# Performance work log

Hardware: AMD Instinct MI355X
Metric: run time of the kernel (lower is better)

The kernel has to match this reference:

```python
import jax, jax.numpy as jnp
import numpy as np

B, S, E, H = 4, 1024, 1024, 16
D = E // H  # head_dim = 64
SCALE = float(np.sqrt(D))


def setup_inputs() -> dict:
    key = jax.random.key(0)
    ks = jax.random.split(key, 12)
    lim = 1.0 / np.sqrt(E)  # torch nn.Linear default init range

    def lin(kw, kb):
        W = jax.random.uniform(kw, (E, E), jnp.float32, -lim, lim)
        b = jax.random.uniform(kb, (E,), jnp.float32, -lim, lim)
        return W, b

    W0, b0 = lin(ks[0], ks[1])
    W1, b1 = lin(ks[2], ks[3])
    W2, b2 = lin(ks[4], ks[5])
    Wv, bv = lin(ks[6], ks[7])
    Wo, bo = lin(ks[8], ks[9])
    A = jax.random.normal(ks[10], (D, D, D), jnp.float32)  # torch.randn core tensor
    x = jax.random.normal(ks[11], (B, S, E), jnp.float32)
    return {"x": x, "W0": W0, "b0": b0, "W1": W1, "b1": b1, "W2": W2, "b2": b2,
            "Wv": Wv, "bv": bv, "Wo": Wo, "bo": bo, "A": A}


def _heads(h):
    # (B,S,E) -> (B,H,S,D)
    return h.reshape(B, S, H, D).transpose(0, 2, 1, 3)


def reference(x, W0, b0, W1, b1, W2, b2, Wv, bv, Wo, bo, A):
    p0 = _heads(x @ W0.T + b0)
    p1 = _heads(x @ W1.T + b1)
    p2 = _heads(x @ W2.T + b2)
    # N=3 multilinear attention score: third projection is contracted over its
    # own sequence index k (faithful to the original einsum construction).
    logits = jnp.einsum('acd,bhia,bhjc,bhkd->bhij', A, p0, p1, p2,
                        optimize=True) / SCALE  # (B,H,S,S)
    attn = jax.nn.softmax(logits, axis=-1)  # dropout inactive (eval / p=0)
    v = _heads(x @ Wv.T + bv)
    values = jnp.einsum('bhij,bhjd->bhid', attn, v)  # (B,H,S,D)
    values = values.transpose(0, 2, 1, 3).reshape(B, S, E)
    out = values @ Wo.T + bo
    return out, attn
```

## Files before the change

kernel.cpp:

```cpp
#include <hip/hip_runtime.h>
#include <hip/hip_bf16.h>
#include <cstddef>

#define B_ 4
#define S_ 1024
#define E_ 1024
#define H_ 16
#define D_ 64
#define BH_ (B_*H_)

typedef __attribute__((ext_vector_type(8))) short short8;
typedef __attribute__((ext_vector_type(4))) float f32x4;
typedef __attribute__((ext_vector_type(4))) unsigned short us4;
typedef unsigned short u16;

__device__ inline u16 f2b(float x) {
    return __builtin_bit_cast(u16, __float2bfloat16(x));
}
__device__ inline float b2f(u16 u) {
    return __bfloat162float(__builtin_bit_cast(__hip_bfloat16, u));
}
__device__ inline void splitf(float x, u16& h, u16& l) {
    h = f2b(x); l = f2b(x - b2f(h));
}

__device__ inline void split_one(const float* __restrict__ in,
                                 u16* __restrict__ oh, u16* __restrict__ ol, int i)
{
    float4 v = ((const float4*)in)[i];
    us4 h, l;
    splitf(v.x, ((u16*)&h)[0], ((u16*)&l)[0]);
    splitf(v.y, ((u16*)&h)[1], ((u16*)&l)[1]);
    splitf(v.z, ((u16*)&h)[2], ((u16*)&l)[2]);
    splitf(v.w, ((u16*)&h)[3], ((u16*)&l)[3]);
    ((us4*)oh)[i] = h;
    ((us4*)ol)[i] = l;
}

__global__ __launch_bounds__(256) void prep(
    const float* __restrict__ x, const float* __restrict__ W0,
    const float* __restrict__ W1, float* __restrict__ xsum_p,
    u16* __restrict__ xh, u16* __restrict__ xl,
    u16* __restrict__ w0h, u16* __restrict__ w0l,
    u16* __restrict__ w1h, u16* __restrict__ w1l)
{
    int bid = blockIdx.x, tid = threadIdx.x;
    if (bid < 4096) {
        split_one(x, xh, xl, bid * 256 + tid);
    } else if (bid < 5120) {
        split_one(W0, w0h, w0l, (bid - 4096) * 256 + tid);
    } else if (bid < 6144) {
        split_one(W1, w1h, w1l, (bid - 5120) * 256 + tid);
    } else {
        int p = bid - 6144;
        int kb = p & 3, b = (p >> 2) & 3, ch = p >> 4;
        int k = kb * 256 + tid;
        const float* base = x + ((size_t)(b * S_ + ch * 64)) * E_ + k;
        float s = 0.f;
#pragma unroll 8
        for (int j = 0; j < 64; ++j) s += base[(size_t)j * E_];
        xsum_p[(ch * 4 + b) * E_ + k] = s;
    }
}

__global__ __launch_bounds__(256) void t2k_M(
    const float* __restrict__ W2, const float* __restrict__ b2v,
    const float* __restrict__ xsum_p, const float* __restrict__ A,
    u16* __restrict__ MTh, u16* __restrict__ MTl)
{
    int h = blockIdx.x, b = blockIdx.y, tid = threadIdx.x;
    __shared__ float xs[1024];
    __shared__ float t2s[64];

#pragma unroll
    for (int j = 0; j < 4; ++j) {
        int k = j * 256 + tid;
        float s = 0.f;
#pragma unroll
        for (int c = 0; c < 16; ++c) s += xsum_p[(c * 4 + b) * E_ + k];
        xs[k] = s;
    }
    __syncthreads();

    int w = tid >> 6, lane = tid & 63;
    for (int nn = w; nn < 64; nn += 4) {
        int n = h * 64 + nn;
        const float* wr = W2 + (size_t)n * E_;
        float s = 0.f;
#pragma unroll
        for (int t = 0; t < 16; ++t) s = fmaf(wr[t * 64 + lane], xs[t * 64 + lane], s);
#pragma unroll
        for (int off = 1; off < 64; off <<= 1) s += __shfl_xor(s, off, 64);
        if (lane == 0) t2s[nn] = s + 1024.0f * b2v[n];
    }
    __syncthreads();

    int bh = b * H_ + h;
    int c = tid & 63;
    int a0 = (tid >> 6) * 16;
    for (int a = a0; a < a0 + 16; ++a) {
        float s = 0.f;
        const float* Ap = A + ((size_t)a * 64 + c) * 64;
#pragma unroll 8
        for (int d = 0; d < 64; ++d) s = fmaf(Ap[d], t2s[d], s);
        u16 hh, ll; splitf(s * 0.125f, hh, ll);
        MTh[(size_t)bh * 4096 + c * 64 + a] = hh;
        MTl[(size_t)bh * 4096 + c * 64 + a] = ll;
    }
}

__global__ __launch_bounds__(256) void gemm_qp1(
    const u16* __restrict__ Xh, const u16* __restrict__ Xl,
    const u16* __restrict__ W0h_, const u16* __restrict__ W0l_,
    const u16* __restrict__ W1h_, const u16* __restrict__ W1l_,
    const float* __restrict__ bias0, const float* __restrict__ bias1,
    const u16* __restrict__ MTh, const u16* __restrict__ MTl,
    u16* __restrict__ qh, u16* __restrict__ ql,
    u16* __restrict__ p1h, u16* __restrict__ p1l)
{
    const int K = 1024;
    __shared__ __align__(16) char smem[40960];
    u16* Xs_h  = (u16*)smem;
    u16* Xs_l  = Xs_h + 128 * 40;
    u16* W0s_h = Xs_l + 128 * 40;
    u16* W0s_l = W0s_h + 64 * 40;
    u16* W1s_h = W0s_l + 64 * 40;
    u16* W1s_l = W1s_h + 64 * 40;
    u16* Cs_h  = (u16*)smem;
    u16* Cs_l  = Cs_h + 128 * 72;

    const int tid = threadIdx.x;
    const int w = tid >> 6, lane = tid & 63;
    const int waveM = w & 1, waveN = w >> 1;
    const int quad = lane >> 4, l16 = lane & 15;
    const int bm = blockIdx.x, bn = blockIdx.y;

    const int xrow = tid >> 1, xko = (tid & 1) * 16;
    const int wrow = tid >> 2, wko = (tid & 3) * 8;

    const u16* xh_g  = Xh  + (size_t)(bm * 128 + xrow) * K + xko;
    const u16* xl_g  = Xl  + (size_t)(bm * 128 + xrow) * K + xko;
    const u16* w0h_g = W0h_ + (size_t)(bn * 64 + wrow) * K + wko;
    const u16* w0l_g = W0l_ + (size_t)(bn * 64 + wrow) * K + wko;
    const u16* w1h_g = W1h_ + (size_t)(bn * 64 + wrow) * K + wko;
    const u16* w1l_g = W1l_ + (size_t)(bn * 64 + wrow) * K + wko;

    f32x4 acc0[4][2] = {};
    f32x4 acc1[4][2] = {};

    for (int k0 = 0; k0 < K; k0 += 32) {
        uint4 xa = *(const uint4*)(xh_g + k0);
        uint4 xb = *(const uint4*)(xh_g + k0 + 8);
        uint4 xc = *(const uint4*)(xl_g + k0);
        uint4 xd = *(const uint4*)(xl_g + k0 + 8);
        uint4 w0a = *(const uint4*)(w0h_g + k0);
        uint4 w0c = *(const uint4*)(w0l_g + k0);
        uint4 w1a = *(const uint4*)(w1h_g + k0);
        uint4 w1c = *(const uint4*)(w1l_g + k0);
        __syncthreads();
        *(uint4*)&Xs_h[xrow * 40 + xko]     = xa;
        *(uint4*)&Xs_h[xrow * 40 + xko + 8] = xb;
        *(uint4*)&Xs_l[xrow * 40 + xko]     = xc;
        *(uint4*)&Xs_l[xrow * 40 + xko + 8] = xd;
        *(uint4*)&W0s_h[wrow * 40 + wko] = w0a;
        *(uint4*)&W0s_l[wrow * 40 + wko] = w0c;
        *(uint4*)&W1s_h[wrow * 40 + wko] = w1a;
        *(uint4*)&W1s_l[wrow * 40 + wko] = w1c;
        __syncthreads();

        short8 ah[4], al[4], b0h[2], b0l[2], b1h[2], b1l[2];
#pragma unroll
        for (int mt = 0; mt < 4; ++mt) {
            int r = (waveM * 64 + mt * 16 + l16) * 40 + quad * 8;
            ah[mt] = *(short8*)&Xs_h[r];
            al[mt] = *(short8*)&Xs_l[r];
        }
#pragma unroll
        for (int nt = 0; nt < 2; ++nt) {
            int r = (waveN * 32 + nt * 16 + l16) * 40 + quad * 8;
            b0h[nt] = *(short8*)&W0s_h[r];
            b0l[nt] = *(short8*)&W0s_l[r];
            b1h[nt] = *(short8*)&W1s_h[r];
            b1l[nt] = *(short8*)&W1s_l[r];
        }
#pragma unroll
        for (int mt = 0; mt < 4; ++mt)
#pragma unroll
            for (int nt = 0; nt < 2; ++nt) {
                acc0[mt][nt] = __builtin_amdgcn_mfma_f32_16x16x32_bf16(ah[mt], b0h[nt], acc0[mt][nt], 0, 0, 0);
                acc1[mt][nt] = __builtin_amdgcn_mfma_f32_16x16x32_bf16(ah[mt], b1h[nt], acc1[mt][nt], 0, 0, 0);
                acc0[mt][nt] = __builtin_amdgcn_mfma_f32_16x16x32_bf16(ah[mt], b0l[nt], acc0[mt][nt], 0, 0, 0);
                acc1[mt][nt] = __builtin_amdgcn_mfma_f32_16x16x32_bf16(ah[mt], b1l[nt], acc1[mt][nt], 0, 0, 0);
                acc0[mt][nt] = __builtin_amdgcn_mfma_f32_16x16x32_bf16(al[mt], b0h[nt], acc0[mt][nt], 0, 0, 0);
                acc1[mt][nt] = __builtin_amdgcn_mfma_f32_16x16x32_bf16(al[mt], b1h[nt], acc1[mt][nt], 0, 0, 0);
            }
    }

    const int bh = (bm >> 3) * H_ + bn;

#pragma unroll
    for (int mt = 0; mt < 4; ++mt)
#pragma unroll
        for (int nt = 0; nt < 2; ++nt)
#pragma unroll
            for (int r = 0; r < 4; ++r) {
                int m = bm * 128 + waveM * 64 + mt * 16 + quad * 4 + r;
                int n = bn * 64 + waveN * 32 + nt * 16 + l16;
                float val = acc1[mt][nt][r] + bias1[n];
                int s = m & 1023, c = n & 63;
                size_t addr = ((size_t)bh * S_ + s) * 64 + c;
                u16 hh, ll; splitf(val, hh, ll);
                p1h[addr] = hh; p1l[addr] = ll;
            }

    __syncthreads();
#pragma unroll
    for (int mt = 0; mt < 4; ++mt)
#pragma unroll
        for (int nt = 0; nt < 2; ++nt)
#pragma unroll
            for (int r = 0; r < 4; ++r) {
                int i = waveM * 64 + mt * 16 + quad * 4 + r;
                int a = waveN * 32 + nt * 16 + l16;
                float val = acc0[mt][nt][r] + bias0[bn * 64 + a];
                u16 hh, ll; splitf(val, hh, ll);
                Cs_h[i * 72 + a] = hh;
                Cs_l[i * 72 + a] = ll;
            }
    __syncthreads();

    const u16* MTh_b = MTh + (size_t)bh * 4096;
    const u16* MTl_b = MTl + (size_t)bh * 4096;
    f32x4 qacc[4][2] = {};
#pragma unroll
    for (int ch = 0; ch < 2; ++ch) {
        short8 mh[2], ml[2];
#pragma unroll
        for (int nt = 0; nt < 2; ++nt) {
            int c = waveN * 32 + nt * 16 + l16;
            mh[nt] = *(const short8*)&MTh_b[c * 64 + ch * 32 + quad * 8];
            ml[nt] = *(const short8*)&MTl_b[c * 64 + ch * 32 + quad * 8];
        }
#pragma unroll
        for (int mt = 0; mt < 4; ++mt) {
            int rr = (waveM * 64 + mt * 16 + l16) * 72 + ch * 32 + quad * 8;
            short8 ca = *(short8*)&Cs_h[rr];
            short8 cl = *(short8*)&Cs_l[rr];
#pragma unroll
            for (int nt = 0; nt < 2; ++nt) {
                qacc[mt][nt] = __builtin_amdgcn_mfma_f32_16x16x32_bf16(ca, mh[nt], qacc[mt][nt], 0, 0, 0);
                qacc[mt][nt] = __builtin_amdgcn_mfma_f32_16x16x32_bf16(ca, ml[nt], qacc[mt][nt], 0, 0, 0);
                qacc[mt][nt] = __builtin_amdgcn_mfma_f32_16x16x32_bf16(cl, mh[nt], qacc[mt][nt], 0, 0, 0);
            }
        }
    }
#pragma unroll
    for (int mt = 0; mt < 4; ++mt)
#pragma unroll
        for (int nt = 0; nt < 2; ++nt)
#pragma unroll
            for (int r = 0; r < 4; ++r) {
                int s = (bm & 7) * 128 + waveM * 64 + mt * 16 + quad * 4 + r;
                int c = waveN * 32 + nt * 16 + l16;
                size_t addr = ((size_t)bh * S_ + s) * 64 + c;
                u16 hh, ll; splitf(qacc[mt][nt][r], hh, ll);
                qh[addr] = hh; ql[addr] = ll;
            }
}

__global__ __launch_bounds__(256) void gemm_plain(
    const u16* __restrict__ Xb, const float* __restrict__ Wf,
    const float* __restrict__ bias, u16* __restrict__ outB,
    float* __restrict__ outF, int mode)
{
    const int K = 1024;
    __shared__ __align__(16) u16 Xs[64 * 40];
    __shared__ __align__(16) u16 Ws[64 * 40];

    const int tid = threadIdx.x;
    const int w = tid >> 6, lane = tid & 63;
    const int waveM = w & 1, waveN = w >> 1;
    const int quad = lane >> 4, l16 = lane & 15;
    const int bm = blockIdx.x, bn = blockIdx.y;
    const int lrow = tid >> 2, lkoff = (tid & 3) * 8;

    const u16* xg = Xb + (size_t)(bm * 64 + lrow) * K + lkoff;
    const float* wg = Wf + (size_t)(bn * 64 + lrow) * K + lkoff;

    f32x4 acc[2][2] = {};

    for (int k0 = 0; k0 < K; k0 += 32) {
        uint4 xv = *(const uint4*)(xg + k0);
        float4 w0 = *(const float4*)(wg + k0);
        float4 w1 = *(const float4*)(wg + k0 + 4);
        short8 wp;
        ((u16*)&wp)[0] = f2b(w0.x); ((u16*)&wp)[1] = f2b(w0.y);
        ((u16*)&wp)[2] = f2b(w0.z); ((u16*)&wp)[3] = f2b(w0.w);
        ((u16*)&wp)[4] = f2b(w1.x); ((u16*)&wp)[5] = f2b(w1.y);
        ((u16*)&wp)[6] = f2b(w1.z); ((u16*)&wp)[7] = f2b(w1.w);
        __syncthreads();
        *(uint4*)&Xs[lrow * 40 + lkoff] = xv;
        *(short8*)&Ws[lrow * 40 + lkoff] = wp;
        __syncthreads();

        short8 af[2], bf_[2];
#pragma unroll
        for (int mt = 0; mt < 2; ++mt)
            af[mt] = *(short8*)&Xs[(waveM * 32 + mt * 16 + l16) * 40 + quad * 8];
#pragma unroll
        for (int nt = 0; nt < 2; ++nt)
            bf_[nt] = *(short8*)&Ws[(waveN * 32 + nt * 16 + l16) * 40 + quad * 8];
#pragma unroll
        for (int mt = 0; mt < 2; ++mt)
#pragma unroll
            for (int nt = 0; nt < 2; ++nt)
                acc[mt][nt] = __builtin_amdgcn_mfma_f32_16x16x32_bf16(af[mt], bf_[nt], acc[mt][nt], 0, 0, 0);
    }

#pragma unroll
    for (int mt = 0; mt < 2; ++mt)
#pragma unroll
        for (int nt = 0; nt < 2; ++nt)
#pragma unroll
            for (int r = 0; r < 4; ++r) {
                int m = bm * 64 + waveM * 32 + mt * 16 + quad * 4 + r;
                int n = bn * 64 + waveN * 32 + nt * 16 + l16;
                float val = acc[mt][nt][r] + bias[n];
                if (mode == 0) {
                    int b = m >> 10, s = m & 1023, h = n >> 6, c = n & 63;
                    outB[((size_t)((b * H_ + h) * 64 + c)) * S_ + s] = f2b(val);
                } else {
                    outF[(size_t)m * 1024 + n] = val;
                }
            }
}

__global__ __launch_bounds__(512) void logits_softmax_pv(
    const u16* __restrict__ qh, const u16* __restrict__ ql,
    const u16* __restrict__ p1h, const u16* __restrict__ p1l,
    const u16* __restrict__ vT, float* __restrict__ attn,
    u16* __restrict__ values)
{
    int bh = blockIdx.x, i0 = blockIdx.y * 32;
    int b = bh >> 4, h = bh & 15;
    int tid = threadIdx.x, w = tid >> 6, lane = tid & 63;
    int quad = lane >> 4, l16 = lane & 15;
    int wg = w >> 2, wj = w & 3;

    __shared__ __align__(16) char sm[60928];
    u16* qhs  = (u16*)sm;
    u16* qls  = (u16*)(sm + 4608);
    u16* p1hs = (u16*)(sm + 9216);
    u16* p1ls = (u16*)(sm + 27648);
    float* redm = (float*)(sm + 46080);
    float* reds = (float*)(sm + 46592);
    u16* Ps  = (u16*)(sm + 9216);
    u16* vs_ = (u16*)(sm + 18432);

    {
        int row = tid >> 4, c0 = (tid & 15) * 4;
        size_t g = ((size_t)bh * S_ + i0 + row) * 64 + c0;
        *(us4*)&qhs[row * 72 + c0] = *(const us4*)&qh[g];
        *(us4*)&qls[row * 72 + c0] = *(const us4*)&ql[g];
    }

    const int jl = tid >> 3, c0s = (tid & 7) * 8;
    const size_t gp = ((size_t)bh * S_ + jl) * 64 + c0s;

    uint4 rha = *(const uint4*)&p1h[gp];
    uint4 rla = *(const uint4*)&p1l[gp];
    *(uint4*)&p1hs[jl * 72 + c0s] = rha;
    *(uint4*)&p1ls[jl * 72 + c0s] = rla;
    uint4 rh1 = *(const uint4*)&p1h[gp + 4096];
    uint4 rl1 = *(const uint4*)&p1l[gp + 4096];
    __syncthreads();

    short8 ah[2], al[2];
#pragma unroll
    for (int ch = 0; ch < 2; ++ch) {
        ah[ch] = *(short8*)&qhs[(wg * 16 + l16) * 72 + ch * 32 + quad * 8];
        al[ch] = *(short8*)&qls[(wg * 16 + l16) * 72 + ch * 32 + quad * 8];
    }

    f32x4 L[16];
    for (int t = 0; t < 16; ++t) {
        int cur = t & 1;
        uint4 rh2, rl2;
        if (t < 14) {
            size_t gn = gp + (size_t)(t + 2) * 4096;
            rh2 = *(const uint4*)&p1h[gn];
            rl2 = *(const uint4*)&p1l[gn];
        }
        int jr = wj * 16 + l16;
        const u16* Hb = &p1hs[cur * 4608 + jr * 72];
        const u16* Lb = &p1ls[cur * 4608 + jr * 72];
        short8 bh0 = *(const short8*)(Hb + quad * 8);
        short8 bh1 = *(const short8*)(Hb + 32 + quad * 8);
        short8 bl0 = *(const short8*)(Lb + quad * 8);
        short8 bl1 = *(const short8*)(Lb + 32 + quad * 8);
        f32x4 a = {};
        a = __builtin_amdgcn_mfma_f32_16x16x32_bf16(ah[0], bh0, a, 0, 0, 0);
        a = __builtin_amdgcn_mfma_f32_16x16x32_bf16(ah[1], bh1, a, 0, 0, 0);
        a = __builtin_amdgcn_mfma_f32_16x16x32_bf16(ah[0], bl0, a, 0, 0, 0);
        a = __builtin_amdgcn_mfma_f32_16x16x32_bf16(ah[1], bl1, a, 0, 0, 0);
        a = __builtin_amdgcn_mfma_f32_16x16x32_bf16(al[0], bh0, a, 0, 0, 0);
        a = __builtin_amdgcn_mfma_f32_16x16x32_bf16(al[1], bh1, a, 0, 0, 0);
        L[t] = a;
        if (t < 15) {
            *(uint4*)&p1hs[(1 - cur) * 4608 + jl * 72 + c0s] = rh1;
            *(uint4*)&p1ls[(1 - cur) * 4608 + jl * 72 + c0s] = rl1;
            if (t < 14) { rh1 = rh2; rl1 = rl2; }
            __syncthreads();
        }
    }

    float mrow[4], srow[4];
#pragma unroll
    for (int r = 0; r < 4; ++r) {
        float m = L[0][r];
#pragma unroll
        for (int t = 1; t < 16; ++t) m = fmaxf(m, L[t][r]);
#pragma unroll
        for (int off = 1; off < 16; off <<= 1) m = fmaxf(m, __shfl_xor(m, off, 64));
        mrow[r] = m;
    }
    if (l16 == 0)
#pragma unroll
        for (int r = 0; r < 4; ++r) redm[wj * 32 + wg * 16 + quad * 4 + r] = mrow[r];
    __syncthreads();
#pragma unroll
    for (int r = 0; r < 4; ++r) {
        int rowg = wg * 16 + quad * 4 + r;
        float m = fmaxf(fmaxf(redm[0 * 32 + rowg], redm[1 * 32 + rowg]),
                        fmaxf(redm[2 * 32 + rowg], redm[3 * 32 + rowg]));
        float s = 0.f;
#pragma unroll
        for (int t = 0; t < 16; ++t) { L[t][r] = __expf(L[t][r] - m); s += L[t][r]; }
#pragma unroll
        for (int off = 1; off < 16; off <<= 1) s += __shfl_xor(s, off, 64);
        srow[r] = s;
    }
    if (l16 == 0)
#pragma unroll
        for (int r = 0; r < 4; ++r) reds[wj * 32 + wg * 16 + quad * 4 + r] = srow[r];
    __syncthreads();
#pragma unroll
    for (int r = 0; r < 4; ++r) {
        int rowg = wg * 16 + quad * 4 + r;
        float inv = 1.0f / (reds[0 * 32 + rowg] + reds[1 * 32 + rowg] +
                            reds[2 * 32 + rowg] + reds[3 * 32 + rowg]);
        float* arow = attn + ((size_t)bh * S_ + i0 + rowg) * S_;
#pragma unroll
        for (int t = 0; t < 16; ++t) {
            float p = L[t][r] * inv;
            L[t][r] = p;
            __builtin_nontemporal_store(p, &arow[t * 64 + wj * 16 + l16]);
        }
    }

    const int dv = tid >> 3, jc = (tid & 7) * 8;
    size_t gv = ((size_t)(bh * 64 + dv)) * S_ + jc;
    uint4 rv = *(const uint4*)&vT[gv];

    f32x4 acc_pv = {};
    for (int t = 0; t < 16; ++t) {
        int cur = t & 1;
#pragma unroll
        for (int r = 0; r < 4; ++r)
            Ps[cur * 2304 + (wg * 16 + quad * 4 + r) * 72 + wj * 16 + l16] = f2b(L[t][r]);
        *(uint4*)&vs_[cur * 4608 + dv * 72 + jc] = rv;
        __syncthreads();
        if (t < 15) rv = *(const uint4*)&vT[gv + (size_t)(t + 1) * 64];
        int d = wj * 16 + l16;
#pragma unroll
        for (int cc = 0; cc < 64; cc += 32) {
            short8 af = *(short8*)&Ps[cur * 2304 + (wg * 16 + l16) * 72 + cc + quad * 8];
            short8 bf = *(short8*)&vs_[cur * 4608 + d * 72 + cc + quad * 8];
            acc_pv = __builtin_amdgcn_mfma_f32_16x16x32_bf16(af, bf, acc_pv, 0, 0, 0);
        }
    }
#pragma unroll
    for (int r = 0; r < 4; ++r) {
        int i = i0 + wg * 16 + quad * 4 + r;
        int d = wj * 16 + l16;
        values[((size_t)(b * S_ + i)) * E_ + h * 64 + d] = f2b(acc_pv[r]);
    }
}

extern "C" void kernel_launch(void* const* d_in, const int* in_sizes, int n_in,
                              void* d_out, int out_size, void* d_ws, size_t ws_size,
                              hipStream_t stream)
{
    const float* x  = (const float*)d_in[0];
    const float* W0 = (const float*)d_in[1];
    const float* b0 = (const float*)d_in[2];
    const float* W1 = (const float*)d_in[3];
    const float* b1 = (const float*)d_in[4];
    const float* W2 = (const float*)d_in[5];
    const float* b2 = (const float*)d_in[6];
    const float* Wv = (const float*)d_in[7];
    const float* bv = (const float*)d_in[8];
    const float* Wo = (const float*)d_in[9];
    const float* bo = (const float*)d_in[10];
    const float* A  = (const float*)d_in[11];

    float* out  = (float*)d_out;
    float* attn = out + (size_t)B_ * S_ * E_;

    u16* xh  = (u16*)d_ws;
    u16* xl  = xh + 4194304;
    u16* w0h = xl + 4194304;
    u16* w0l = w0h + 1048576;
    u16* w1h = w0l + 1048576;
    u16* w1l = w1h + 1048576;
    u16* p1h = w1l + 1048576;
    u16* p1l = p1h + 4194304;
    u16* qh  = p1l + 4194304;
    u16* ql  = qh + 4194304;
    u16* vT  = ql + 4194304;
    u16* values = vT + 4194304;
    u16* MTh = values + 4194304;
    u16* MTl = MTh + 262144;
    float* xsum_p = (float*)p1h;

    prep<<<6400, 256, 0, stream>>>(x, W0, W1, xsum_p, xh, xl, w0h, w0l, w1h, w1l);
    t2k_M<<<dim3(16, 4), 256, 0, stream>>>(W2, b2, xsum_p, A, MTh, MTl);

    gemm_qp1<<<dim3(32, 16), 256, 0, stream>>>(xh, xl, w0h, w0l, w1h, w1l,
                                               b0, b1, MTh, MTl, qh, ql, p1h, p1l);

    dim3 gp(64, 16);
    gemm_plain<<<gp, 256, 0, stream>>>(xh, Wv, bv, vT, nullptr, 0);

    logits_softmax_pv<<<dim3(64, 32), 512, 0, stream>>>(qh, ql, p1h, p1l, vT, attn, values);

    gemm_plain<<<gp, 256, 0, stream>>>(values, Wo, bo, nullptr, out, 1);
}
```

Measured before the change: 607.6 us.

## Merge Q/P1 and V GEMMs into one launch, pre-convert weights, double PV step

Wv and Wo are now converted to bf16 once in the prep kernel, so the plain GEMMs no longer convert fp32 weights inside their K loops. The plain GEMM tile grows to 128 rows. The V projection runs in the same launch as the Q/P1 GEMM, one block-index range each, so both fill the device together. The PV loop in the attention kernel now handles two 64-column tiles per barrier, halving the synchronisations, and shared memory is re-laid out to fit the larger buffers. Costs are extra workspace, reuse of the values buffer to hold Wv in bf16, and mixed block types in one grid.

```diff
diff --git a/kernel.cpp b/kernel.cpp
--- a/kernel.cpp
+++ b/kernel.cpp
@@ -37,12 +37,24 @@
     ((us4*)ol)[i] = l;
 }
 
+__device__ inline void conv_one(const float* __restrict__ in,
+                                u16* __restrict__ ob, int i)
+{
+    float4 v = ((const float4*)in)[i];
+    us4 h;
+    ((u16*)&h)[0] = f2b(v.x); ((u16*)&h)[1] = f2b(v.y);
+    ((u16*)&h)[2] = f2b(v.z); ((u16*)&h)[3] = f2b(v.w);
+    ((us4*)ob)[i] = h;
+}
+
 __global__ __launch_bounds__(256) void prep(
     const float* __restrict__ x, const float* __restrict__ W0,
-    const float* __restrict__ W1, float* __restrict__ xsum_p,
+    const float* __restrict__ W1, const float* __restrict__ Wv,
+    const float* __restrict__ Wo, float* __restrict__ xsum_p,
     u16* __restrict__ xh, u16* __restrict__ xl,
     u16* __restrict__ w0h, u16* __restrict__ w0l,
-    u16* __restrict__ w1h, u16* __restrict__ w1l)
+    u16* __restrict__ w1h, u16* __restrict__ w1l,
+    u16* __restrict__ wvb, u16* __restrict__ wob)
 {
     int bid = blockIdx.x, tid = threadIdx.x;
     if (bid < 4096) {
@@ -51,8 +63,12 @@
         split_one(W0, w0h, w0l, (bid - 4096) * 256 + tid);
     } else if (bid < 6144) {
         split_one(W1, w1h, w1l, (bid - 5120) * 256 + tid);
+    } else if (bid < 7168) {
+        conv_one(Wv, wvb, (bid - 6144) * 256 + tid);
+    } else if (bid < 8192) {
+        conv_one(Wo, wob, (bid - 7168) * 256 + tid);
     } else {
-        int p = bid - 6144;
+        int p = bid - 8192;
         int kb = p & 3, b = (p >> 2) & 3, ch = p >> 4;
         int k = kb * 256 + tid;
         const float* base = x + ((size_t)(b * S_ + ch * 64)) * E_ + k;
@@ -109,17 +125,17 @@
     }
 }
 
-__global__ __launch_bounds__(256) void gemm_qp1(
+__device__ void qp1_body(
     const u16* __restrict__ Xh, const u16* __restrict__ Xl,
     const u16* __restrict__ W0h_, const u16* __restrict__ W0l_,
     const u16* __restrict__ W1h_, const u16* __restrict__ W1l_,
     const float* __restrict__ bias0, const float* __restrict__ bias1,
     const u16* __restrict__ MTh, const u16* __restrict__ MTl,
     u16* __restrict__ qh, u16* __restrict__ ql,
-    u16* __restrict__ p1h, u16* __restrict__ p1l)
+    u16* __restrict__ p1h, u16* __restrict__ p1l,
+    int bm, int bn, char* smem)
 {
     const int K = 1024;
-    __shared__ __align__(16) char smem[40960];
     u16* Xs_h  = (u16*)smem;
     u16* Xs_l  = Xs_h + 128 * 40;
     u16* W0s_h = Xs_l + 128 * 40;
@@ -133,7 +149,6 @@
     const int w = tid >> 6, lane = tid & 63;
     const int waveM = w & 1, waveN = w >> 1;
     const int quad = lane >> 4, l16 = lane & 15;
-    const int bm = blockIdx.x, bn = blockIdx.y;
 
     const int xrow = tid >> 1, xko = (tid & 1) * 16;
     const int wrow = tid >> 2, wko = (tid & 3) * 8;
@@ -268,62 +283,58 @@
             }
 }
 
-__global__ __launch_bounds__(256) void gemm_plain(
-    const u16* __restrict__ Xb, const float* __restrict__ Wf,
+__device__ void plain128_body(
+    const u16* __restrict__ Xb, const u16* __restrict__ Wb,
     const float* __restrict__ bias, u16* __restrict__ outB,
-    float* __restrict__ outF, int mode)
+    float* __restrict__ outF, int mode, int bm, int bn, char* smem)
 {
     const int K = 1024;
-    __shared__ __align__(16) u16 Xs[64 * 40];
-    __shared__ __align__(16) u16 Ws[64 * 40];
+    u16* Xs = (u16*)smem;
+    u16* Ws = Xs + 128 * 40;
 
     const int tid = threadIdx.x;
     const int w = tid >> 6, lane = tid & 63;
     const int waveM = w & 1, waveN = w >> 1;
     const int quad = lane >> 4, l16 = lane & 15;
-    const int bm = blockIdx.x, bn = blockIdx.y;
-    const int lrow = tid >> 2, lkoff = (tid & 3) * 8;
-
-    const u16* xg = Xb + (size_t)(bm * 64 + lrow) * K + lkoff;
-    const float* wg = Wf + (size_t)(bn * 64 + lrow) * K + lkoff;
-
-    f32x4 acc[2][2] = {};
+    const int xrow = tid >> 1, xko = (tid & 1) * 16;
+    const int wrow = tid >> 2, wko = (tid & 3) * 8;
+
+    const u16* xg = Xb + (size_t)(bm * 128 + xrow) * K + xko;
+    const u16* wg = Wb + (size_t)(bn * 64 + wrow) * K + wko;
+
+    f32x4 acc[4][2] = {};
 
     for (int k0 = 0; k0 < K; k0 += 32) {
-        uint4 xv = *(const uint4*)(xg + k0);
-        float4 w0 = *(const float4*)(wg + k0);
-        float4 w1 = *(const float4*)(wg + k0 + 4);
-        short8 wp;
-        ((u16*)&wp)[0] = f2b(w0.x); ((u16*)&wp)[1] = f2b(w0.y);
-        ((u16*)&wp)[2] = f2b(w0.z); ((u16*)&wp)[3] = f2b(w0.w);
-        ((u16*)&wp)[4] = f2b(w1.x); ((u16*)&wp)[5] = f2b(w1.y);
-        ((u16*)&wp)[6] = f2b(w1.z); ((u16*)&wp)[7] = f2b(w1.w);
+        uint4 xa = *(const uint4*)(xg + k0);
+        uint4 xb = *(const uint4*)(xg + k0 + 8);
+        uint4 wa = *(const uint4*)(wg + k0);
         __syncthreads();
-        *(uint4*)&Xs[lrow * 40 + lkoff] = xv;
-        *(short8*)&Ws[lrow * 40 + lkoff] = wp;
+        *(uint4*)&Xs[xrow * 40 + xko]     = xa;
+        *(uint4*)&Xs[xrow * 40 + xko + 8] = xb;
+        *(uint4*)&Ws[wrow * 40 + wko]     = wa;
         __syncthreads();
 
-        short8 af[2], bf_[2];
-#pragma unroll
-        for (int mt = 0; mt < 2; ++mt)
-            af[mt] = *(short8*)&Xs[(waveM * 32 + mt * 16 + l16) * 40 + quad * 8];
+        short8 af[4], bf_[2];
+#pragma unroll
+        for (int mt = 0; mt < 4; ++mt)
+            af[mt] = *(short8*)&Xs[(waveM * 64 + mt * 16 + l16) * 40 + quad * 8];
 #pragma unroll
         for (int nt = 0; nt < 2; ++nt)
             bf_[nt] = *(short8*)&Ws[(waveN * 32 + nt * 16 + l16) * 40 + quad * 8];
 #pragma unroll
-        for (int mt = 0; mt < 2; ++mt)
+        for (int mt = 0; mt < 4; ++mt)
 #pragma unroll
             for (int nt = 0; nt < 2; ++nt)
                 acc[mt][nt] = __builtin_amdgcn_mfma_f32_16x16x32_bf16(af[mt], bf_[nt], acc[mt][nt], 0, 0, 0);
     }
 
 #pragma unroll
-    for (int mt = 0; mt < 2; ++mt)
+    for (int mt = 0; mt < 4; ++mt)
 #pragma unroll
         for (int nt = 0; nt < 2; ++nt)
 #pragma unroll
             for (int r = 0; r < 4; ++r) {
-                int m = bm * 64 + waveM * 32 + mt * 16 + quad * 4 + r;
+                int m = bm * 128 + waveM * 64 + mt * 16 + quad * 4 + r;
                 int n = bn * 64 + waveN * 32 + nt * 16 + l16;
                 float val = acc[mt][nt][r] + bias[n];
                 if (mode == 0) {
@@ -335,6 +346,36 @@
             }
 }
 
+__global__ __launch_bounds__(256) void gemm_mid(
+    const u16* __restrict__ xh, const u16* __restrict__ xl,
+    const u16* __restrict__ w0h, const u16* __restrict__ w0l,
+    const u16* __restrict__ w1h, const u16* __restrict__ w1l,
+    const float* __restrict__ b0, const float* __restrict__ b1,
+    const u16* __restrict__ MTh, const u16* __restrict__ MTl,
+    u16* __restrict__ qh, u16* __restrict__ ql,
+    u16* __restrict__ p1h, u16* __restrict__ p1l,
+    const u16* __restrict__ wvb, const float* __restrict__ bv,
+    u16* __restrict__ vT)
+{
+    __shared__ __align__(16) char smem[40960];
+    int bid = blockIdx.x;
+    if (bid < 512) {
+        qp1_body(xh, xl, w0h, w0l, w1h, w1l, b0, b1, MTh, MTl,
+                 qh, ql, p1h, p1l, bid & 31, bid >> 5, smem);
+    } else {
+        int b2 = bid - 512;
+        plain128_body(xh, wvb, bv, vT, nullptr, 0, b2 & 31, b2 >> 5, smem);
+    }
+}
+
+__global__ __launch_bounds__(256) void gemm_fin(
+    const u16* __restrict__ values, const u16* __restrict__ wob,
+    const float* __restrict__ bo, float* __restrict__ out)
+{
+    __shared__ __align__(16) char smem[15360];
+    plain128_body(values, wob, bo, nullptr, out, 1, blockIdx.x, blockIdx.y, smem);
+}
+
 __global__ __launch_bounds__(512) void logits_softmax_pv(
     const u16* __restrict__ qh, const u16* __restrict__ ql,
     const u16* __restrict__ p1h, const u16* __restrict__ p1l,
@@ -347,14 +388,14 @@
     int quad = lane >> 4, l16 = lane & 15;
     int wg = w >> 2, wj = w & 3;
 
-    __shared__ __align__(16) char sm[60928];
+    __shared__ __align__(16) char sm[56320];
     u16* qhs  = (u16*)sm;
     u16* qls  = (u16*)(sm + 4608);
     u16* p1hs = (u16*)(sm + 9216);
     u16* p1ls = (u16*)(sm + 27648);
-    float* redm = (float*)(sm + 46080);
-    float* reds = (float*)(sm + 46592);
-    u16* Ps  = (u16*)(sm + 9216);
+    float* redm = (float*)(sm + 55296);
+    float* reds = (float*)(sm + 55808);
+    u16* Ps  = (u16*)sm;
     u16* vs_ = (u16*)(sm + 18432);
 
     {
@@ -459,30 +500,41 @@
     }
 
     const int dv = tid >> 3, jc = (tid & 7) * 8;
-    size_t gv = ((size_t)(bh * 64 + dv)) * S_ + jc;
-    uint4 rv = *(const uint4*)&vT[gv];
+    const size_t gv = (size_t)(bh * 64 + dv) * S_;
+    uint4 rv0 = *(const uint4*)&vT[gv + jc];
+    uint4 rv1 = *(const uint4*)&vT[gv + 64 + jc];
 
     f32x4 acc_pv = {};
-    for (int t = 0; t < 16; ++t) {
-        int cur = t & 1;
-#pragma unroll
-        for (int r = 0; r < 4; ++r)
-            Ps[cur * 2304 + (wg * 16 + quad * 4 + r) * 72 + wj * 16 + l16] = f2b(L[t][r]);
-        *(uint4*)&vs_[cur * 4608 + dv * 72 + jc] = rv;
+    const int d = wj * 16 + l16;
+    for (int tt = 0; tt < 8; ++tt) {
+        int cur = tt & 1;
+        u16* Pb = Ps + cur * 4608;
+        u16* Vb = vs_ + cur * 9216;
+#pragma unroll
+        for (int r = 0; r < 4; ++r) {
+            int pr = (wg * 16 + quad * 4 + r) * 72 + wj * 16 + l16;
+            Pb[pr]        = f2b(L[2 * tt][r]);
+            Pb[2304 + pr] = f2b(L[2 * tt + 1][r]);
+        }
+        *(uint4*)&Vb[dv * 72 + jc]        = rv0;
+        *(uint4*)&Vb[4608 + dv * 72 + jc] = rv1;
         __syncthreads();
-        if (t < 15) rv = *(const uint4*)&vT[gv + (size_t)(t + 1) * 64];
-        int d = wj * 16 + l16;
-#pragma unroll
-        for (int cc = 0; cc < 64; cc += 32) {
-            short8 af = *(short8*)&Ps[cur * 2304 + (wg * 16 + l16) * 72 + cc + quad * 8];
-            short8 bf = *(short8*)&vs_[cur * 4608 + d * 72 + cc + quad * 8];
-            acc_pv = __builtin_amdgcn_mfma_f32_16x16x32_bf16(af, bf, acc_pv, 0, 0, 0);
-        }
+        if (tt < 7) {
+            rv0 = *(const uint4*)&vT[gv + (size_t)(2 * tt + 2) * 64 + jc];
+            rv1 = *(const uint4*)&vT[gv + (size_t)(2 * tt + 3) * 64 + jc];
+        }
+#pragma unroll
+        for (int tp = 0; tp < 2; ++tp)
+#pragma unroll
+            for (int cc = 0; cc < 64; cc += 32) {
+                short8 af = *(short8*)&Pb[tp * 2304 + (wg * 16 + l16) * 72 + cc + quad * 8];
+                short8 bf = *(short8*)&Vb[tp * 4608 + d * 72 + cc + quad * 8];
+                acc_pv = __builtin_amdgcn_mfma_f32_16x16x32_bf16(af, bf, acc_pv, 0, 0, 0);
+            }
     }
 #pragma unroll
     for (int r = 0; r < 4; ++r) {
         int i = i0 + wg * 16 + quad * 4 + r;
-        int d = wj * 16 + l16;
         values[((size_t)(b * S_ + i)) * E_ + h * 64 + d] = f2b(acc_pv[r]);
     }
 }
@@ -521,18 +573,19 @@
     u16* values = vT + 4194304;
     u16* MTh = values + 4194304;
     u16* MTl = MTh + 262144;
+    u16* wob = MTl + 262144;
     float* xsum_p = (float*)p1h;
-
-    prep<<<6400, 256, 0, stream>>>(x, W0, W1, xsum_p, xh, xl, w0h, w0l, w1h, w1l);
+    u16* wvb = values;
+
+    prep<<<8448, 256, 0, stream>>>(x, W0, W1, Wv, Wo, xsum_p,
+                                   xh, xl, w0h, w0l, w1h, w1l, wvb, wob);
     t2k_M<<<dim3(16, 4), 256, 0, stream>>>(W2, b2, xsum_p, A, MTh, MTl);
 
-    gemm_qp1<<<dim3(32, 16), 256, 0, stream>>>(xh, xl, w0h, w0l, w1h, w1l,
-                                               b0, b1, MTh, MTl, qh, ql, p1h, p1l);
-
-    dim3 gp(64, 16);
-    gemm_plain<<<gp, 256, 0, stream>>>(xh, Wv, bv, vT, nullptr, 0);
+    gemm_mid<<<1024, 256, 0, stream>>>(xh, xl, w0h, w0l, w1h, w1l,
+                                       b0, b1, MTh, MTl, qh, ql, p1h, p1l,
+                                       wvb, bv, vT);
 
     logits_softmax_pv<<<dim3(64, 32), 512, 0, stream>>>(qh, ql, p1h, p1l, vT, attn, values);
 
-    gemm_plain<<<gp, 256, 0, stream>>>(values, Wo, bo, nullptr, out, 1);
-}
+    gemm_fin<<<dim3(32, 16), 256, 0, stream>>>(values, wob, bo, out);
+}
```

New measurement: 537.7 us. 11.5% less time.
